# Performance work log

Hardware: AMD Instinct MI355X
Metric: run time of the kernel (lower is better)

The kernel has to match this reference:

```python
import jax, jax.numpy as jnp
import numpy as np

NEG_SLOPE = 0.2  # PyG GATConv default negative_slope


def gat_layer(x, src, dst, N, W, att_src, att_dst, bias, heads, out_ch, concat):
    # x: [N, Fin]; W: [Fin, heads*out_ch]; att_*: [heads, out_ch]; bias matches output dim
    h = (x @ W).reshape(N, heads, out_ch)              # [N, H, C]
    a_src = (h * att_src).sum(-1)                      # [N, H]
    a_dst = (h * att_dst).sum(-1)                      # [N, H]
    e = jax.nn.leaky_relu(a_src[src] + a_dst[dst], NEG_SLOPE)  # [E, H]
    # segment softmax over incoming edges of each destination node
    e_max = jax.ops.segment_max(e, dst, num_segments=N)        # [N, H]
    e_exp = jnp.exp(e - e_max[dst])                             # [E, H]
    denom = jax.ops.segment_sum(e_exp, dst, num_segments=N)    # [N, H]
    alpha = e_exp / (denom[dst] + 1e-16)                        # [E, H]
    msg = alpha[:, :, None] * h[src]                            # [E, H, C]
    out = jax.ops.segment_sum(msg, dst, num_segments=N)        # [N, H, C]
    out = out.reshape(N, heads * out_ch) if concat else out.mean(axis=1)
    return out + bias


def setup_inputs() -> dict:
    key = jax.random.key(0)
    ks = jax.random.split(key, 10)
    N, E = 40000, 160000
    Fin, H1, C1 = 602, 8, 256
    H2, C2 = 1, 42
    g = lambda k, shape, fan: (jax.random.normal(k, shape, dtype=jnp.float32) * (1.0 / np.sqrt(fan)))
    return {
        "x": jax.random.normal(ks[0], (N, Fin), dtype=jnp.float32),
        "edge_index": jax.random.randint(ks[1], (2, E), 0, N, dtype=jnp.int64),
        "W1": g(ks[2], (Fin, H1 * C1), Fin),
        "att_src1": g(ks[3], (H1, C1), C1),
        "att_dst1": g(ks[4], (H1, C1), C1),
        "b1": jnp.zeros((H1 * C1,), dtype=jnp.float32),
        "W2": g(ks[5], (H1 * C1, H2 * C2), H1 * C1),
        "att_src2": g(ks[6], (H2, C2), C2),
        "att_dst2": g(ks[7], (H2, C2), C2),
        "b2": jnp.zeros((C2,), dtype=jnp.float32),
    }


def reference(x, edge_index, W1, att_src1, att_dst1, b1, W2, att_src2, att_dst2, b2):
    N = x.shape[0]
    # PyG GATConv default add_self_loops=True
    loops = jnp.arange(N, dtype=edge_index.dtype)
    src = jnp.concatenate([edge_index[0], loops])
    dst = jnp.concatenate([edge_index[1], loops])
    h = gat_layer(x, src, dst, N, W1, att_src1, att_dst1, b1, heads=8, out_ch=256, concat=True)
    h = jax.nn.relu(h)  # dropout is identity in eval mode
    h = gat_layer(h, src, dst, N, W2, att_src2, att_dst2, b2, heads=1, out_ch=42, concat=False)
    return jax.nn.log_softmax(h, axis=1)
```

## Files before the change

### kernel.cpp

```cpp
#include <hip/hip_runtime.h>
#include <hip/hip_bf16.h>

#define NN   40000
#define NE   160000
#define ETOT 200000
#define FIN  602
#define NH1  8
#define C1   256
#define F1   2048
#define C2   42
#define NEG  0.2f
#define NB   157
#define KP   608
#define MP   40192
#define CSS  264

typedef unsigned short u16;
typedef unsigned int   u32;
typedef __bf16 bf16x8 __attribute__((ext_vector_type(8)));
typedef float  f32x4  __attribute__((ext_vector_type(4)));

__device__ __forceinline__ float bfu(u16 v){ return __uint_as_float(((u32)v) << 16); }
__device__ __forceinline__ float bflo(u32 u){ return __uint_as_float(u << 16); }
__device__ __forceinline__ float bfhi(u32 u){ return __uint_as_float(u & 0xffff0000u); }
__device__ __forceinline__ u16 f2bf(float f){
  u32 u = __float_as_uint(f);
  u32 r = (u + 0x7fffu + ((u >> 16) & 1u)) >> 16;
  return (u16)r;
}

__device__ __forceinline__ void gl_lds16(const u16* g, u16* l) {
  __builtin_amdgcn_global_load_lds(
      (const __attribute__((address_space(1))) u32*)(g),
      (__attribute__((address_space(3))) u32*)(l), 16, 0, 0);
}

__global__ void probe_k(const u32* __restrict__ xw, const int* __restrict__ ei,
                        int* __restrict__ flags) {
  if (threadIdx.x == 0) {
    int zc = 0;
    for (int k = 0; k < 64; ++k) zc += (ei[2*k + 1] == 0) ? 1 : 0;
    flags[0] = (zc == 64) ? 1 : 0;
    int inr = 0;
    for (int k = 0; k < 64; ++k) {
      u32 low = xw[k] & 0xffffu;
      int e = (int)((low >> 7) & 0xff);
      inr += (e >= 100 && e <= 140) ? 1 : 0;
    }
    flags[1] = (inr >= 32) ? 0 : 1;
  }
}

__global__ void cvt_all_k(const void* __restrict__ as1, const void* __restrict__ ad1,
                          const void* __restrict__ b1,  const void* __restrict__ as2,
                          const void* __restrict__ ad2, const void* __restrict__ b2,
                          float* __restrict__ as1c, float* __restrict__ ad1c,
                          float* __restrict__ b1c,  float* __restrict__ as2c,
                          float* __restrict__ ad2c, float* __restrict__ b2c,
                          const int* __restrict__ flags) {
  int i = blockIdx.x * 256 + threadIdx.x;
  int fm = flags[1];
  if (i < F1) {
    as1c[i] = fm ? ((const float*)as1)[i] : bfu(((const u16*)as1)[i]);
    ad1c[i] = fm ? ((const float*)ad1)[i] : bfu(((const u16*)ad1)[i]);
    b1c[i]  = fm ? ((const float*)b1)[i]  : bfu(((const u16*)b1)[i]);
  }
  if (i < C2) {
    as2c[i] = fm ? ((const float*)as2)[i] : bfu(((const u16*)as2)[i]);
    ad2c[i] = fm ? ((const float*)ad2)[i] : bfu(((const u16*)ad2)[i]);
    b2c[i]  = fm ? ((const float*)b2)[i]  : bfu(((const u16*)b2)[i]);
  }
}

__global__ __launch_bounds__(192) void xb4_k(const void* __restrict__ x, u16* __restrict__ xb,
                                             const int* __restrict__ flags) {
  int t = threadIdx.x;
  if (t >= 152) return;
  int row = blockIdx.x;
  int k0 = t * 4;
  ushort4 o = make_ushort4(0, 0, 0, 0);
  if (row < NN) {
    if (k0 + 4 <= FIN) {
      if (flags[1]) {
        const float* xp = (const float*)x + (size_t)row * FIN + k0;
        float2 p0 = *(const float2*)(xp);
        float2 p1 = *(const float2*)(xp + 2);
        o.x = f2bf(p0.x); o.y = f2bf(p0.y); o.z = f2bf(p1.x); o.w = f2bf(p1.y);
      } else {
        const u16* xp = (const u16*)x + (size_t)row * FIN + k0;
        u32 p0 = *(const u32*)(xp);
        u32 p1 = *(const u32*)(xp + 2);
        o.x = (u16)(p0 & 0xffff); o.y = (u16)(p0 >> 16);
        o.z = (u16)(p1 & 0xffff); o.w = (u16)(p1 >> 16);
      }
    } else {
      u16 e[4] = {0, 0, 0, 0};
      for (int q = 0; q < 4; ++q) {
        int k = k0 + q;
        if (k < FIN)
          e[q] = flags[1] ? f2bf(((const float*)x)[(size_t)row * FIN + k])
                          : ((const u16*)x)[(size_t)row * FIN + k];
      }
      o = make_ushort4(e[0], e[1], e[2], e[3]);
    }
  }
  *(ushort4*)(xb + (size_t)row * KP + k0) = o;
}

__global__ void w1t_k(const void* __restrict__ W1, u16* __restrict__ w1t,
                      const int* __restrict__ flags) {
  int n = blockIdx.x * 256 + threadIdx.x;
  int k = blockIdx.y;
  if (n >= F1) return;
  u16 v = 0;
  if (k < FIN) v = flags[1] ? f2bf(((const float*)W1)[(size_t)k * F1 + n])
                            : ((const u16*)W1)[(size_t)k * F1 + n];
  w1t[(size_t)n * KP + k] = v;
}

__global__ void w2t_k(const void* __restrict__ W2, u16* __restrict__ w2t,
                      const int* __restrict__ flags) {
  int i = blockIdx.x * 256 + threadIdx.x;
  if (i >= 64 * F1) return;
  int c = i >> 11, k = i & (F1 - 1);
  u16 v = 0;
  if (c < C2) v = flags[1] ? f2bf(((const float*)W2)[(size_t)k * C2 + c])
                           : ((const u16*)W2)[(size_t)k * C2 + c];
  w2t[i] = v;
}

__device__ __forceinline__ void edge_sd(const int* __restrict__ ei, int e, int imode,
                                        int& s, int& d) {
  if (e < NE) {
    if (imode) { s = ei[2*e]; d = ei[2*(NE + e)]; }
    else       { s = ei[e];   d = ei[NE + e];     }
  } else { s = d = e - NE; }
}

__global__ void deg_k(const int* __restrict__ ei, int* __restrict__ deg,
                      const int* __restrict__ flags) {
  int e = blockIdx.x * 256 + threadIdx.x;
  if (e >= ETOT) return;
  int s, d; edge_sd(ei, e, flags[0], s, d);
  atomicAdd(&deg[d], 1);
}

__global__ __launch_bounds__(256) void scan1_k(const int* __restrict__ deg,
                                               int* __restrict__ tmp, int* __restrict__ bsum) {
  __shared__ int s[256];
  int b = blockIdx.x, t = threadIdx.x, i = b * 256 + t;
  int v = (i < NN) ? deg[i] : 0;
  s[t] = v; __syncthreads();
  for (int o = 1; o < 256; o <<= 1) {
    int u = (t >= o) ? s[t - o] : 0;
    __syncthreads(); s[t] += u; __syncthreads();
  }
  if (i < NN) tmp[i] = s[t];
  if (t == 255) bsum[b] = s[255];
}

__global__ __launch_bounds__(256) void scan2_k(int* __restrict__ bsum) {
  __shared__ int s[256];
  int t = threadIdx.x;
  int v = (t < NB) ? bsum[t] : 0;
  s[t] = v; __syncthreads();
  for (int o = 1; o < 256; o <<= 1) {
    int u = (t >= o) ? s[t - o] : 0;
    __syncthreads(); s[t] += u; __syncthreads();
  }
  if (t < NB) bsum[t] = s[t];
}

__global__ void scan3_k(const int* __restrict__ deg, const int* __restrict__ tmp,
                        const int* __restrict__ bsum, int* __restrict__ start, int* __restrict__ cur) {
  int i = blockIdx.x * 256 + threadIdx.x;
  if (i >= NN) return;
  int b = i >> 8;
  int off = b ? bsum[b - 1] : 0;
  int excl = tmp[i] - deg[i] + off;
  start[i] = excl; cur[i] = excl;
}

__global__ void fill_k(const int* __restrict__ ei, int* __restrict__ cur,
                       int* __restrict__ csr_src, int* __restrict__ csr_dst,
                       const int* __restrict__ flags) {
  int e = blockIdx.x * 256 + threadIdx.x;
  if (e >= ETOT) return;
  int s, d; edge_sd(ei, e, flags[0], s, d);
  int pos = atomicAdd(&cur[d], 1);
  csr_src[pos] = s; csr_dst[pos] = d;
}

__global__ __launch_bounds__(512) void gemm1c_k(const u16* __restrict__ xb,
                                                const u16* __restrict__ w1t,
                                                u16* __restrict__ h1,
                                                const float* __restrict__ as1c,
                                                const float* __restrict__ ad1c,
                                                float* __restrict__ a_s1,
                                                float* __restrict__ a_d1) {
  __shared__ u16 As[3 * 8192];
  __shared__ u16 Bs[3 * 8192];
  const int t = threadIdx.x;
  const int lane = t & 63, wid = t >> 6;
  const int wr = wid >> 2, wc = wid & 3;
  const int m0 = blockIdx.y * 256, n0 = blockIdx.x * 256;
  const int l16 = lane & 15;
  f32x4 acc[8][4];
  #pragma unroll
  for (int i = 0; i < 8; ++i)
    #pragma unroll
    for (int j = 0; j < 4; ++j) acc[i][j] = (f32x4){0.f, 0.f, 0.f, 0.f};

  const int kc = ((t & 3) ^ ((t >> 3) & 3)) * 8;
  const size_t sa0 = (size_t)(m0 + (t >> 2)) * KP + kc;
  const size_t sa1 = sa0 + (size_t)128 * KP;
  const size_t sb0 = (size_t)(n0 + (t >> 2)) * KP + kc;
  const size_t sb1 = sb0 + (size_t)128 * KP;

  const int fsw = ((lane >> 4) ^ ((l16 >> 1) & 3)) << 3;
  const int rdA = (wr * 128 + l16) * 32 + fsw;
  const int rdB = (wc * 64 + l16) * 32 + fsw;

#define STAGE(K0, B) do {                                  \
    u16* a_ = As + (B) * 8192 + (wid << 9);                \
    u16* b_ = Bs + (B) * 8192 + (wid << 9);                \
    gl_lds16(xb  + sa0 + (K0), a_);                        \
    gl_lds16(xb  + sa1 + (K0), a_ + 4096);                 \
    gl_lds16(w1t + sb0 + (K0), b_);                        \
    gl_lds16(w1t + sb1 + (K0), b_ + 4096);                 \
  } while (0)

  STAGE(0, 0);
  STAGE(32, 1);
  int bi = 0;
  for (int k0 = 0; k0 < KP; k0 += 32) {
    const int steps_left = (KP - k0) >> 5;
    if (steps_left > 2) {
      int bn = bi + 2; bn = (bn >= 3) ? bn - 3 : bn;
      STAGE(k0 + 64, bn);
      asm volatile("s_waitcnt vmcnt(8)" ::: "memory");
    } else if (steps_left == 2) {
      asm volatile("s_waitcnt vmcnt(4)" ::: "memory");
    } else {
      asm volatile("s_waitcnt vmcnt(0)" ::: "memory");
    }
    __builtin_amdgcn_s_barrier();
    const u16* Ab = As + bi * 8192;
    const u16* Bb = Bs + bi * 8192;
    bf16x8 bfr[4];
    #pragma unroll
    for (int ni = 0; ni < 4; ++ni)
      bfr[ni] = *(const bf16x8*)&Bb[rdB + ni * 512];
    #pragma unroll
    for (int mi = 0; mi < 8; ++mi) {
      bf16x8 af = *(const bf16x8*)&Ab[rdA + mi * 512];
      #pragma unroll
      for (int ni = 0; ni < 4; ++ni)
        acc[mi][ni] = __builtin_amdgcn_mfma_f32_16x16x32_bf16(af, bfr[ni], acc[mi][ni], 0, 0, 0);
    }
    __builtin_amdgcn_s_barrier();
    bi = bi + 1; bi = (bi >= 3) ? 0 : bi;
  }
#undef STAGE

  const int h0 = n0 >> 8;
  const int lr4 = (lane >> 4) * 4;
  #pragma unroll
  for (int mi = 0; mi < 8; ++mi) {
    float ps[4] = {0.f, 0.f, 0.f, 0.f}, pd[4] = {0.f, 0.f, 0.f, 0.f};
    #pragma unroll
    for (int ni = 0; ni < 4; ++ni) {
      int col = n0 + wc * 64 + ni * 16 + l16;
      float wsv = as1c[col], wdv = ad1c[col];
      #pragma unroll
      for (int r = 0; r < 4; ++r) {
        float v = acc[mi][ni][r];
        ps[r] += v * wsv;
        pd[r] += v * wdv;
      }
    }
    #pragma unroll
    for (int o = 1; o < 16; o <<= 1) {
      #pragma unroll
      for (int r = 0; r < 4; ++r) {
        ps[r] += __shfl_xor(ps[r], o, 64);
        pd[r] += __shfl_xor(pd[r], o, 64);
      }
    }
    if (l16 == 0) {
      int rowb = m0 + wr * 128 + mi * 16 + lr4;
      #pragma unroll
      for (int r = 0; r < 4; ++r) {
        int row = rowb + r;
        if (row < NN) {
          atomicAdd(&a_s1[row * NH1 + h0], ps[r]);
          atomicAdd(&a_d1[row * NH1 + h0], pd[r]);
        }
      }
    }
  }

  u16* Cs = As;
  const int rrow = t >> 4;
  const int rchk = t & 15;
  for (int mi = 0; mi < 8; ++mi) {
    __syncthreads();
    #pragma unroll
    for (int ni = 0; ni < 4; ++ni)
      #pragma unroll
      for (int r = 0; r < 4; ++r)
        Cs[(wr * 16 + lr4 + r) * CSS + wc * 64 + ni * 16 + l16] = f2bf(acc[mi][ni][r]);
    __syncthreads();
    int grow = m0 + (rrow >> 4) * 128 + mi * 16 + (rrow & 15);
    if (grow < NN) {
      const uint4* src = (const uint4*)&Cs[rrow * CSS + rchk * 16];
      uint4 v0 = src[0], v1 = src[1];
      uint4* dst = (uint4*)&h1[(size_t)grow * F1 + n0 + rchk * 16];
      dst[0] = v0; dst[1] = v1;
    }
  }
}

__global__ __launch_bounds__(256) void gemm1m_k(const void* __restrict__ xv,
                                                const u16* __restrict__ w1t,
                                                u16* __restrict__ h1,
                                                const int* __restrict__ flags) {
  __shared__ u16 As[128][40];
  __shared__ u16 Bs[128][40];
  const int fm = flags[1];
  const int t = threadIdx.x;
  const int lane = t & 63, wid = t >> 6;
  const int wr = wid >> 1, wc = wid & 1;
  const int m0 = blockIdx.y * 128, n0 = blockIdx.x * 128;
  const int l16 = lane & 15, lk = (lane >> 4) * 8;
  f32x4 acc[4][4];
  #pragma unroll
  for (int i = 0; i < 4; ++i)
    #pragma unroll
    for (int j = 0; j < 4; ++j) acc[i][j] = (f32x4){0.f, 0.f, 0.f, 0.f};
  const int arow = t >> 2;
  const int akb  = (t & 3) * 8;
  for (int k0 = 0; k0 < KP; k0 += 32) {
    #pragma unroll
    for (int i = 0; i < 2; ++i) {
      int row = arow + i * 64;
      int rg = m0 + row;
      u32 d0 = 0, d1 = 0, d2 = 0, d3 = 0;
      if (rg < NN) {
        if (k0 + 32 <= FIN) {
          if (fm) {
            const float* xp = (const float*)xv + (size_t)rg * FIN + k0 + akb;
            float2 p0 = *(const float2*)(xp);
            float2 p1 = *(const float2*)(xp + 2);
            float2 p2 = *(const float2*)(xp + 4);
            float2 p3 = *(const float2*)(xp + 6);
            d0 = (u32)f2bf(p0.x) | ((u32)f2bf(p0.y) << 16);
            d1 = (u32)f2bf(p1.x) | ((u32)f2bf(p1.y) << 16);
            d2 = (u32)f2bf(p2.x) | ((u32)f2bf(p2.y) << 16);
            d3 = (u32)f2bf(p3.x) | ((u32)f2bf(p3.y) << 16);
          } else {
            const u16* xp = (const u16*)xv + (size_t)rg * FIN + k0 + akb;
            d0 = *(const u32*)(xp);
            d1 = *(const u32*)(xp + 2);
            d2 = *(const u32*)(xp + 4);
            d3 = *(const u32*)(xp + 6);
          }
        } else {
          u16 e[8];
          #pragma unroll
          for (int q = 0; q < 8; ++q) {
            int k = k0 + akb + q;
            e[q] = 0;
            if (k < FIN)
              e[q] = fm ? f2bf(((const float*)xv)[(size_t)rg * FIN + k])
                        : ((const u16*)xv)[(size_t)rg * FIN + k];
          }
          d0 = (u32)e[0] | ((u32)e[1] << 16);
          d1 = (u32)e[2] | ((u32)e[3] << 16);
          d2 = (u32)e[4] | ((u32)e[5] << 16);
          d3 = (u32)e[6] | ((u32)e[7] << 16);
        }
      }
      *(uint4*)&As[row][akb] = make_uint4(d0, d1, d2, d3);
      const u16* wp = w1t + (size_t)(n0 + row) * KP + k0 + akb;
      *(uint4*)&Bs[row][akb] = *(const uint4*)wp;
    }
    __syncthreads();
    bf16x8 bfr[4];
    #pragma unroll
    for (int ni = 0; ni < 4; ++ni)
      bfr[ni] = *(const bf16x8*)&Bs[wc * 64 + ni * 16 + l16][lk];
    #pragma unroll
    for (int mi = 0; mi < 4; ++mi) {
      bf16x8 af = *(const bf16x8*)&As[wr * 64 + mi * 16 + l16][lk];
      #pragma unroll
      for (int ni = 0; ni < 4; ++ni)
        acc[mi][ni] = __builtin_amdgcn_mfma_f32_16x16x32_bf16(af, bfr[ni], acc[mi][ni], 0, 0, 0);
    }
    __syncthreads();
  }
  const int lr4 = (lane >> 4) * 4;
  #pragma unroll
  for (int mi = 0; mi < 4; ++mi) {
    #pragma unroll
    for (int r = 0; r < 4; ++r) {
      int row = m0 + wr * 64 + mi * 16 + lr4 + r;
      if (row < NN) {
        #pragma unroll
        for (int ni = 0; ni < 4; ++ni) {
          int col = n0 + wc * 64 + ni * 16 + l16;
          h1[(size_t)row * F1 + col] = f2bf(acc[mi][ni][r]);
        }
      }
    }
  }
}

__global__ __launch_bounds__(256) void att1_k(const u16* __restrict__ h1,
                                              const float* __restrict__ as1c, const float* __restrict__ ad1c,
                                              float* __restrict__ a_s, float* __restrict__ a_d) {
  int n = blockIdx.x, t = threadIdx.x;
  int h = t >> 5, l = t & 31;
  int base = h * C1 + l * 8;
  const u16* hp = h1 + (size_t)n * F1 + base;
  uint4 v = *(const uint4*)hp;
  u32 w[4] = {v.x, v.y, v.z, v.w};
  float ss = 0.f, sd = 0.f;
  #pragma unroll
  for (int p = 0; p < 4; ++p) {
    float e0 = bflo(w[p]), e1 = bfhi(w[p]);
    ss += e0 * as1c[base + 2*p] + e1 * as1c[base + 2*p + 1];
    sd += e0 * ad1c[base + 2*p] + e1 * ad1c[base + 2*p + 1];
  }
  #pragma unroll
  for (int o = 16; o > 0; o >>= 1) {
    ss += __shfl_down(ss, o, 32);
    sd += __shfl_down(sd, o, 32);
  }
  if (l == 0) { a_s[n * NH1 + h] = ss; a_d[n * NH1 + h] = sd; }
}

__global__ __launch_bounds__(512) void gfuse_k(const int* __restrict__ start, const int* __restrict__ deg,
                                               const int* __restrict__ csr_src,
                                               const float* __restrict__ a_s1, const float* __restrict__ a_d1,
                                               const u16* __restrict__ h1, const float* __restrict__ b1c,
                                               const u16* __restrict__ w2t,
                                               const float* __restrict__ as2c, const float* __restrict__ ad2c,
                                               float* __restrict__ h2,
                                               float* __restrict__ a_s2, float* __restrict__ a_d2) {
  __shared__ u16 rowsL[16 * F1];
  __shared__ float pb[4][16][16];
  int t = threadIdx.x;
  int nb = blockIdx.x * 16;
  int sub = t & 255, grp = t >> 8;
  int h = sub >> 5;
  int c0 = sub * 8;
  float4 bA = *(const float4*)(b1c + c0);
  float4 bB = *(const float4*)(b1c + c0 + 4);
  for (int ii = 0; ii < 8; ++ii) {
    int i = grp * 8 + ii;
    int n = nb + i;
    int s0 = start[n], jend = s0 + deg[n];
    float ad = a_d1[n * NH1 + h];
    float a0=0.f,a1=0.f,a2=0.f,a3=0.f,a4=0.f,a5=0.f,a6=0.f,a7=0.f,den=0.f;
    int j = s0;
    for (; j + 2 <= jend; j += 2) {
      int sA = csr_src[j], sB = csr_src[j + 1];
      float vA = a_s1[sA * NH1 + h] + ad;
      float vB = a_s1[sB * NH1 + h] + ad;
      vA = vA > 0.f ? vA : NEG * vA;
      vB = vB > 0.f ? vB : NEG * vB;
      float eA = expf(vA), eB = expf(vB);
      uint4 uA = *(const uint4*)(h1 + (size_t)sA * F1 + c0);
      uint4 uB = *(const uint4*)(h1 + (size_t)sB * F1 + c0);
      den += eA + eB;
      a0 += eA * bflo(uA.x) + eB * bflo(uB.x);
      a1 += eA * bfhi(uA.x) + eB * bfhi(uB.x);
      a2 += eA * bflo(uA.y) + eB * bflo(uB.y);
      a3 += eA * bfhi(uA.y) + eB * bfhi(uB.y);
      a4 += eA * bflo(uA.z) + eB * bflo(uB.z);
      a5 += eA * bfhi(uA.z) + eB * bfhi(uB.z);
      a6 += eA * bflo(uA.w) + eB * bflo(uB.w);
      a7 += eA * bfhi(uA.w) + eB * bfhi(uB.w);
    }
    if (j < jend) {
      int sA = csr_src[j];
      float vA = a_s1[sA * NH1 + h] + ad;
      vA = vA > 0.f ? vA : NEG * vA;
      float eA = expf(vA);
      uint4 uA = *(const uint4*)(h1 + (size_t)sA * F1 + c0);
      den += eA;
      a0 += eA * bflo(uA.x); a1 += eA * bfhi(uA.x);
      a2 += eA * bflo(uA.y); a3 += eA * bfhi(uA.y);
      a4 += eA * bflo(uA.z); a5 += eA * bfhi(uA.z);
      a6 += eA * bflo(uA.w); a7 += eA * bfhi(uA.w);
    }
    float inv = 1.f / (den + 1e-16f);
    u16 o0 = f2bf(fmaxf(a0 * inv + bA.x, 0.f));
    u16 o1 = f2bf(fmaxf(a1 * inv + bA.y, 0.f));
    u16 o2 = f2bf(fmaxf(a2 * inv + bA.z, 0.f));
    u16 o3 = f2bf(fmaxf(a3 * inv + bA.w, 0.f));
    u16 o4 = f2bf(fmaxf(a4 * inv + bB.x, 0.f));
    u16 o5 = f2bf(fmaxf(a5 * inv + bB.y, 0.f));
    u16 o6 = f2bf(fmaxf(a6 * inv + bB.z, 0.f));
    u16 o7 = f2bf(fmaxf(a7 * inv + bB.w, 0.f));
    uint4 pk;
    pk.x = (u32)o0 | ((u32)o1 << 16);
    pk.y = (u32)o2 | ((u32)o3 << 16);
    pk.z = (u32)o4 | ((u32)o5 << 16);
    pk.w = (u32)o6 | ((u32)o7 << 16);
    int sw = (i & 7) << 3;
    *(uint4*)&rowsL[i * F1 + (c0 ^ sw)] = pk;
  }
  __syncthreads();
  int lane = t & 63, wid = t >> 6;
  int g = wid & 3, kh = wid >> 2;
  int l16 = lane & 15, lk = (lane >> 4) * 8;
  const u16* wt = w2t + (size_t)(g * 16 + l16) * F1;
  int sw = (l16 & 7) << 3;
  f32x4 acc2 = (f32x4){0.f, 0.f, 0.f, 0.f};
  const int kbase = kh * (F1 / 2);
  for (int k0 = 0; k0 < F1 / 2; k0 += 32) {
    int kk = kbase + k0 + lk;
    bf16x8 af = *(const bf16x8*)&rowsL[l16 * F1 + (kk ^ sw)];
    bf16x8 bf = *(const bf16x8*)(wt + kk);
    acc2 = __builtin_amdgcn_mfma_f32_16x16x32_bf16(af, bf, acc2, 0, 0, 0);
  }
  int mb = (lane >> 4) * 4;
  if (kh == 1) {
    #pragma unroll
    for (int r = 0; r < 4; ++r) pb[g][mb + r][l16] = acc2[r];
  }
  __syncthreads();
  if (kh == 0) {
    int col = g * 16 + l16;
    float vals[4];
    #pragma unroll
    for (int r = 0; r < 4; ++r) vals[r] = acc2[r] + pb[g][mb + r][l16];
    if (col < C2) {
      #pragma unroll
      for (int r = 0; r < 4; ++r)
        h2[(size_t)(nb + mb + r) * C2 + col] = vals[r];
    }
    float as2v = (col < C2) ? as2c[col] : 0.f;
    float ad2v = (col < C2) ? ad2c[col] : 0.f;
    float ps[4], pd[4];
    #pragma unroll
    for (int r = 0; r < 4; ++r) { ps[r] = vals[r] * as2v; pd[r] = vals[r] * ad2v; }
    #pragma unroll
    for (int o = 1; o < 16; o <<= 1) {
      #pragma unroll
      for (int r = 0; r < 4; ++r) {
        ps[r] += __shfl_xor(ps[r], o, 64);
        pd[r] += __shfl_xor(pd[r], o, 64);
      }
    }
    if (l16 == 0 && g < 3) {
      #pragma unroll
      for (int r = 0; r < 4; ++r) {
        atomicAdd(&a_s2[nb + mb + r], ps[r]);
        atomicAdd(&a_d2[nb + mb + r], pd[r]);
      }
    }
  }
}

__global__ __launch_bounds__(256) void gath2_k(const int* __restrict__ start, const int* __restrict__ deg,
                                               const int* __restrict__ csr_src,
                                               const float* __restrict__ a_s, const float* __restrict__ a_d,
                                               const float* __restrict__ h2, const float* __restrict__ b2,
                                               void* __restrict__ outv, const int* __restrict__ flags) {
  int w = threadIdx.x >> 6, lane = threadIdx.x & 63;
  int n = blockIdx.x * 4 + w;
  int s0 = start[n], cnt = deg[n];
  float ad = a_d[n];
  float acc = 0.f, den = 0.f;
  for (int j = s0; j < s0 + cnt; ++j) {
    int s = csr_src[j];
    float v = a_s[s] + ad;
    v = v > 0.f ? v : NEG * v;
    float e = expf(v);
    den += e;
    if (lane < C2) acc += e * h2[(size_t)s * C2 + lane];
  }
  float raw = (lane < C2) ? acc / (den + 1e-16f) + b2[lane] : -1e30f;
  float m = raw;
  #pragma unroll
  for (int o = 32; o > 0; o >>= 1) m = fmaxf(m, __shfl_down(m, o, 64));
  m = __shfl(m, 0, 64);
  float e2 = (lane < C2) ? expf(raw - m) : 0.f;
  float ssum = e2;
  #pragma unroll
  for (int o = 32; o > 0; o >>= 1) ssum += __shfl_down(ssum, o, 64);
  ssum = __shfl(ssum, 0, 64);
  if (lane < C2) {
    float v = raw - m - logf(ssum);
    if (flags[1]) ((float*)outv)[(size_t)n * C2 + lane] = v;
    else          ((u16*) outv)[(size_t)n * C2 + lane] = f2bf(v);
  }
}

extern "C" void kernel_launch(void* const* d_in, const int* in_sizes, int n_in,
                              void* d_out, int out_size, void* d_ws, size_t ws_size,
                              hipStream_t stream) {
  const void* x   = d_in[0];
  const int*  ei  = (const int*)d_in[1];
  const void* W1  = d_in[2];
  const void* as1 = d_in[3];
  const void* ad1 = d_in[4];
  const void* b1  = d_in[5];
  const void* W2  = d_in[6];
  const void* as2 = d_in[7];
  const void* ad2 = d_in[8];
  const void* b2  = d_in[9];

  char* ws = (char*)d_ws;
  u16*   h1      = (u16*)  (ws);
  float* h2      = (float*)(ws + 163840000);
  float* a_s1    = (float*)(ws + 170560000);
  float* a_d1    = (float*)(ws + 171840000);
  float* a_s2    = (float*)(ws + 173120000);
  float* a_d2    = (float*)(ws + 173280000);
  int*   deg     = (int*)  (ws + 173440000);
  int*   start   = (int*)  (ws + 173600000);
  int*   cur     = (int*)  (ws + 173760000);
  int*   tmp     = (int*)  (ws + 173920000);
  int*   csr_src = (int*)  (ws + 174080000);
  int*   csr_dst = (int*)  (ws + 174880000);
  int*   bsum    = (int*)  (ws + 175680000);
  u16*   w1t     = (u16*)  (ws + 175681024);
  u16*   w2t     = (u16*)  (ws + 178171392);
  float* as1c    = (float*)(ws + 178433536);
  float* ad1c    = (float*)(ws + 178441728);
  float* b1c     = (float*)(ws + 178449920);
  float* as2c    = (float*)(ws + 178458112);
  float* ad2c    = (float*)(ws + 178458368);
  float* b2c     = (float*)(ws + 178458624);
  int*   flags   = (int*)  (ws + 178458880);
  const size_t TOTAL_BASE = 178459136;
  u16*   xb      = (u16*)  (ws + TOTAL_BASE);
  const size_t TOTAL_A = TOTAL_BASE + (size_t)MP * KP * 2;
  if (ws_size < TOTAL_BASE) return;
  const bool pathA = (ws_size >= TOTAL_A);

  probe_k<<<1, 64, 0, stream>>>((const u32*)x, ei, flags);

  cvt_all_k<<<(F1 + 255) / 256, 256, 0, stream>>>(as1, ad1, b1, as2, ad2, b2,
                                                  as1c, ad1c, b1c, as2c, ad2c, b2c, flags);
  w1t_k<<<dim3(8, KP), 256, 0, stream>>>(W1, w1t, flags);
  w2t_k<<<(64 * F1 + 255) / 256, 256, 0, stream>>>(W2, w2t, flags);

  hipMemsetAsync(deg, 0, NN * sizeof(int), stream);
  hipMemsetAsync(a_s1, 0, (2 * NN * NH1 + 2 * NN) * sizeof(float), stream);
  const int EB = (ETOT + 255) / 256;
  deg_k  <<<EB, 256, 0, stream>>>(ei, deg, flags);
  scan1_k<<<NB, 256, 0, stream>>>(deg, tmp, bsum);
  scan2_k<<<1, 256, 0, stream>>>(bsum);
  scan3_k<<<NB, 256, 0, stream>>>(deg, tmp, bsum, start, cur);
  fill_k <<<EB, 256, 0, stream>>>(ei, cur, csr_src, csr_dst, flags);

  if (pathA) {
    xb4_k<<<MP, 192, 0, stream>>>(x, xb, flags);
    gemm1c_k<<<dim3(8, MP / 256), 512, 0, stream>>>(xb, w1t, h1, as1c, ad1c, a_s1, a_d1);
  } else {
    gemm1m_k<<<dim3(16, 313), 256, 0, stream>>>(x, w1t, h1, flags);
    att1_k<<<NN, 256, 0, stream>>>(h1, as1c, ad1c, a_s1, a_d1);
  }
  gfuse_k<<<NN / 16, 512, 0, stream>>>(start, deg, csr_src, a_s1, a_d1, h1, b1c, w2t,
                                       as2c, ad2c, h2, a_s2, a_d2);

  gath2_k<<<NN / 4, 256, 0, stream>>>(start, deg, csr_src, a_s2, a_d2, h2, b2c, d_out, flags);
}
```

Measured before the change: 618.3 us.

## Switch GEMM1 to double-buffered LDS and unroll edge aggregation by four

The GEMM1 main loop drops from a three-stage LDS ring with explicit vmcnt waits to a simpler two-buffer ping-pong that uses __syncthreads, which cuts LDS use and may raise occupancy but leaves less prefetch depth to hide global latency. Separately, the gfuse edge loop is unrolled from two to four edges per iteration through a macro, so more gathers are in flight at once, with a scalar remainder loop. The GEMM change can expose load latency because the compiler-inserted waits before the barrier wait for everything outstanding, including the prefetch that was just issued.

```diff
diff --git a/kernel.cpp b/kernel.cpp
--- a/kernel.cpp
+++ b/kernel.cpp
@@ -198,8 +198,8 @@
                                                 const float* __restrict__ ad1c,
                                                 float* __restrict__ a_s1,
                                                 float* __restrict__ a_d1) {
-  __shared__ u16 As[3 * 8192];
-  __shared__ u16 Bs[3 * 8192];
+  __shared__ u16 As[2 * 8192];
+  __shared__ u16 Bs[2 * 8192];
   const int t = threadIdx.x;
   const int lane = t & 63, wid = t >> 6;
   const int wr = wid >> 2, wc = wid & 3;
@@ -231,22 +231,12 @@
   } while (0)
 
   STAGE(0, 0);
-  STAGE(32, 1);
-  int bi = 0;
+  __syncthreads();
+  int cur = 0;
   for (int k0 = 0; k0 < KP; k0 += 32) {
-    const int steps_left = (KP - k0) >> 5;
-    if (steps_left > 2) {
-      int bn = bi + 2; bn = (bn >= 3) ? bn - 3 : bn;
-      STAGE(k0 + 64, bn);
-      asm volatile("s_waitcnt vmcnt(8)" ::: "memory");
-    } else if (steps_left == 2) {
-      asm volatile("s_waitcnt vmcnt(4)" ::: "memory");
-    } else {
-      asm volatile("s_waitcnt vmcnt(0)" ::: "memory");
-    }
-    __builtin_amdgcn_s_barrier();
-    const u16* Ab = As + bi * 8192;
-    const u16* Bb = Bs + bi * 8192;
+    if (k0 + 32 < KP) STAGE(k0 + 32, cur ^ 1);
+    const u16* Ab = As + cur * 8192;
+    const u16* Bb = Bs + cur * 8192;
     bf16x8 bfr[4];
     #pragma unroll
     for (int ni = 0; ni < 4; ++ni)
@@ -258,8 +248,8 @@
       for (int ni = 0; ni < 4; ++ni)
         acc[mi][ni] = __builtin_amdgcn_mfma_f32_16x16x32_bf16(af, bfr[ni], acc[mi][ni], 0, 0, 0);
     }
-    __builtin_amdgcn_s_barrier();
-    bi = bi + 1; bi = (bi >= 3) ? 0 : bi;
+    __syncthreads();
+    cur ^= 1;
   }
 #undef STAGE
 
@@ -440,6 +430,19 @@
   if (l == 0) { a_s[n * NH1 + h] = ss; a_d[n * NH1 + h] = sd; }
 }
 
+#define EDGE_ACC(S)                                                   \
+  do {                                                                \
+    float v_ = a_s1[(S) * NH1 + h] + ad;                              \
+    v_ = v_ > 0.f ? v_ : NEG * v_;                                    \
+    float e_ = expf(v_);                                              \
+    uint4 u_ = *(const uint4*)(h1 + (size_t)(S) * F1 + c0);           \
+    den += e_;                                                        \
+    a0 += e_ * bflo(u_.x); a1 += e_ * bfhi(u_.x);                     \
+    a2 += e_ * bflo(u_.y); a3 += e_ * bfhi(u_.y);                     \
+    a4 += e_ * bflo(u_.z); a5 += e_ * bfhi(u_.z);                     \
+    a6 += e_ * bflo(u_.w); a7 += e_ * bfhi(u_.w);                     \
+  } while (0)
+
 __global__ __launch_bounds__(512) void gfuse_k(const int* __restrict__ start, const int* __restrict__ deg,
                                                const int* __restrict__ csr_src,
                                                const float* __restrict__ a_s1, const float* __restrict__ a_d1,
@@ -464,36 +467,14 @@
     float ad = a_d1[n * NH1 + h];
     float a0=0.f,a1=0.f,a2=0.f,a3=0.f,a4=0.f,a5=0.f,a6=0.f,a7=0.f,den=0.f;
     int j = s0;
-    for (; j + 2 <= jend; j += 2) {
-      int sA = csr_src[j], sB = csr_src[j + 1];
-      float vA = a_s1[sA * NH1 + h] + ad;
-      float vB = a_s1[sB * NH1 + h] + ad;
-      vA = vA > 0.f ? vA : NEG * vA;
-      vB = vB > 0.f ? vB : NEG * vB;
-      float eA = expf(vA), eB = expf(vB);
-      uint4 uA = *(const uint4*)(h1 + (size_t)sA * F1 + c0);
-      uint4 uB = *(const uint4*)(h1 + (size_t)sB * F1 + c0);
-      den += eA + eB;
-      a0 += eA * bflo(uA.x) + eB * bflo(uB.x);
-      a1 += eA * bfhi(uA.x) + eB * bfhi(uB.x);
-      a2 += eA * bflo(uA.y) + eB * bflo(uB.y);
-      a3 += eA * bfhi(uA.y) + eB * bfhi(uB.y);
-      a4 += eA * bflo(uA.z) + eB * bflo(uB.z);
-      a5 += eA * bfhi(uA.z) + eB * bfhi(uB.z);
-      a6 += eA * bflo(uA.w) + eB * bflo(uB.w);
-      a7 += eA * bfhi(uA.w) + eB * bfhi(uB.w);
-    }
-    if (j < jend) {
+    for (; j + 4 <= jend; j += 4) {
+      int sA = csr_src[j],     sB = csr_src[j + 1];
+      int sC = csr_src[j + 2], sD = csr_src[j + 3];
+      EDGE_ACC(sA); EDGE_ACC(sB); EDGE_ACC(sC); EDGE_ACC(sD);
+    }
+    for (; j < jend; ++j) {
       int sA = csr_src[j];
-      float vA = a_s1[sA * NH1 + h] + ad;
-      vA = vA > 0.f ? vA : NEG * vA;
-      float eA = expf(vA);
-      uint4 uA = *(const uint4*)(h1 + (size_t)sA * F1 + c0);
-      den += eA;
-      a0 += eA * bflo(uA.x); a1 += eA * bfhi(uA.x);
-      a2 += eA * bflo(uA.y); a3 += eA * bfhi(uA.y);
-      a4 += eA * bflo(uA.z); a5 += eA * bfhi(uA.z);
-      a6 += eA * bflo(uA.w); a7 += eA * bfhi(uA.w);
+      EDGE_ACC(sA);
     }
     float inv = 1.f / (den + 1e-16f);
     u16 o0 = f2bf(fmaxf(a0 * inv + bA.x, 0.f));
```

After: 589.0 us. 1.05x faster.
